# Kernel optimization log

Hardware: AMD Instinct MI355X
Metric: run time of the kernel (lower is better)

## Reference

```python
import jax, jax.numpy as jnp
import numpy as np

N_NODES = 100000
N_EDGES = 3200000
IN_DIM = 128
HID = 128
K = 20  # n_gaussians


def gcn_conv(x, src, dst, W, b, n_nodes):
    """PyG GCNConv: add self-loops, symmetric normalization, linear transform.
    out = D^{-1/2} (A + I) D^{-1/2} (x @ W) + b, where D is degree of A+I.
    """
    h = x @ W  # [N, out_dim]
    # degree on A + I (self-loop contributes 1 to every node)
    deg = jax.ops.segment_sum(jnp.ones_like(dst, dtype=h.dtype), dst,
                              num_segments=n_nodes) + 1.0
    dis = jax.lax.rsqrt(deg)  # deg >= 1, safe
    norm = dis[src] * dis[dst]  # [E]
    # gather -> scale -> scatter-add (edges), plus self-loop term dis_i^2 * h_i
    agg = jax.ops.segment_sum(h[src] * norm[:, None], dst,
                              num_segments=n_nodes)
    agg = agg + h * (dis * dis)[:, None]
    return agg + b


def setup_inputs() -> dict:
    key = jax.random.key(0)
    ks = jax.random.split(key, 12)
    x = jax.random.normal(ks[0], (N_NODES, IN_DIM), dtype=jnp.float32)
    edge_index = jax.random.randint(ks[1], (2, N_EDGES), 0, N_NODES, dtype=jnp.int32)
    s = 1.0 / np.sqrt(HID)
    W1 = jax.random.uniform(ks[2], (IN_DIM, HID), jnp.float32, -s, s)
    b1 = jnp.zeros((HID,), jnp.float32)
    W2 = jax.random.uniform(ks[3], (HID, HID), jnp.float32, -s, s)
    b2 = jnp.zeros((HID,), jnp.float32)
    pi_W = jax.random.uniform(ks[4], (HID, K), jnp.float32, -s, s)
    pi_b = jnp.zeros((K,), jnp.float32)
    mu_W = jax.random.uniform(ks[5], (HID, K), jnp.float32, -s, s)
    mu_b = jnp.zeros((K,), jnp.float32)
    ls_W = jax.random.uniform(ks[6], (HID, K), jnp.float32, -s, s)
    ls_b = jnp.zeros((K,), jnp.float32)
    return {"x": x, "edge_index": edge_index, "W1": W1, "b1": b1,
            "W2": W2, "b2": b2, "pi_W": pi_W, "pi_b": pi_b,
            "mu_W": mu_W, "mu_b": mu_b, "ls_W": ls_W, "ls_b": ls_b}


def reference(x, edge_index, W1, b1, W2, b2, pi_W, pi_b, mu_W, mu_b, ls_W, ls_b):
    src, dst = edge_index[0], edge_index[1]
    n = x.shape[0]
    h = jax.nn.relu(gcn_conv(x, src, dst, W1, b1, n))
    h = jax.nn.relu(gcn_conv(h, src, dst, W2, b2, n))
    pi = jax.nn.softmax(h @ pi_W + pi_b, axis=1)
    mu = h @ mu_W + mu_b
    log_sigma = h @ ls_W + ls_b
    return (pi, mu, log_sigma)
```

## Files before the change

kernel.cpp:

```cpp
#include <hip/hip_runtime.h>
#include <hip/hip_fp16.h>
#include <cstdint>
#include <cstddef>

#define IN_DIM 128
#define HID    128
#define NG     20
#define T      4096
#define MAXB   400

typedef _Float16 half8 __attribute__((ext_vector_type(8)));
typedef _Float16 half4 __attribute__((ext_vector_type(4)));
typedef float    f32x4 __attribute__((ext_vector_type(4)));

__global__ void zero_ints(int* __restrict__ a, int n) {
  int i = blockIdx.x * blockDim.x + threadIdx.x;
  if (i < n) a[i] = 0;
}

__global__ __launch_bounds__(512) void binsort1(const int* __restrict__ src,
    const int* __restrict__ dst, int* __restrict__ tmp, int* __restrict__ bofs,
    int* __restrict__ bintot, int NBC, int E) {
  __shared__ int lhist[MAXB];
  __shared__ int lscan[512];
  __shared__ int lcur[MAXB];
  __shared__ int sbuf[T];
  int tid = threadIdx.x;
  int tile0 = blockIdx.x * T;
  int m = E - tile0; if (m > T) m = T;

  for (int i = tid; i < NBC; i += 512) lhist[i] = 0;
  __syncthreads();

  int dreg[8];
#pragma unroll
  for (int j = 0; j < 8; ++j) {
    int idx = j * 512 + tid;
    dreg[j] = -1;
    if (idx < m) {
      int d = dst[tile0 + idx];
      dreg[j] = d;
      atomicAdd(&lhist[d >> 8], 1);
    }
  }
  __syncthreads();

  int v = (tid < NBC) ? lhist[tid] : 0;
  lscan[tid] = v;
  __syncthreads();
  for (int o = 1; o < 512; o <<= 1) {
    int t = (tid >= o) ? lscan[tid - o] : 0;
    __syncthreads();
    lscan[tid] += t;
    __syncthreads();
  }
  if (tid < NBC) lcur[tid] = lscan[tid] - v;
  __syncthreads();

  int ST = NBC + 1;
  for (int i = tid; i < NBC; i += 512) bofs[(size_t)blockIdx.x * ST + i] = lcur[i];
  if (tid == 0) bofs[(size_t)blockIdx.x * ST + NBC] = m;
  for (int i = tid; i < NBC; i += 512)
    if (lhist[i]) atomicAdd(&bintot[i], lhist[i]);
  __syncthreads();

#pragma unroll
  for (int j = 0; j < 8; ++j) {
    int idx = j * 512 + tid;
    if (idx < m) {
      int d = dreg[j];
      int s = src[tile0 + idx];
      int slot = atomicAdd(&lcur[d >> 8], 1);
      sbuf[slot] = ((d & 255) << 17) | s;
    }
  }
  __syncthreads();

  int nv = m >> 2;
  int4* out4 = (int4*)(tmp + tile0);
  const int4* sb4 = (const int4*)sbuf;
  for (int i = tid; i < nv; i += 512) out4[i] = sb4[i];
  for (int i = (nv << 2) + tid; i < m; i += 512) tmp[tile0 + i] = sbuf[i];
}

__global__ __launch_bounds__(512) void binscan(const int* __restrict__ bintot,
                                               int* __restrict__ binbase, int NBC) {
  __shared__ int s[512];
  int tid = threadIdx.x;
  int v = (tid < NBC) ? bintot[tid] : 0;
  s[tid] = v;
  __syncthreads();
  for (int o = 1; o < 512; o <<= 1) {
    int t = (tid >= o) ? s[tid - o] : 0;
    __syncthreads();
    s[tid] += t;
    __syncthreads();
  }
  if (tid < NBC) binbase[tid] = s[tid] - v;
}

__global__ __launch_bounds__(1024) void binsort2(const int* __restrict__ tmp,
    const int* __restrict__ bofs, const int* __restrict__ binbase,
    int* __restrict__ csrc, int* __restrict__ cnt, float* __restrict__ dis,
    int* __restrict__ offs, int NBC, int nblk, int N) {
  __shared__ int lcnt[256];
  __shared__ int lsc[256];
  __shared__ int lcur2[256];
  int b = blockIdx.x;
  int tid = threadIdx.x;
  if (tid < 256) lcnt[tid] = 0;
  __syncthreads();
  int ST = NBC + 1;
  for (int r = tid; r < nblk; r += 1024) {
    int s = bofs[(size_t)r * ST + b];
    int e2 = bofs[(size_t)r * ST + b + 1];
    int base = r * T;
    for (int k = s; k < e2; ++k)
      atomicAdd(&lcnt[tmp[base + k] >> 17], 1);
  }
  __syncthreads();
  if (tid < 256) lsc[tid] = lcnt[tid];
  __syncthreads();
  for (int o = 1; o < 256; o <<= 1) {
    int t = 0;
    if (tid < 256 && tid >= o) t = lsc[tid - o];
    __syncthreads();
    if (tid < 256) lsc[tid] += t;
    __syncthreads();
  }
  int gbase = binbase[b];
  if (tid < 256) {
    int excl = lsc[tid] - lcnt[tid];
    lcur2[tid] = gbase + excl;
    int node = (b << 8) + tid;
    if (node < N) {
      cnt[node] = lcnt[tid];
      dis[node] = rsqrtf((float)lcnt[tid] + 1.0f);
      offs[node] = gbase + excl;
    }
  }
  __syncthreads();
  for (int r = tid; r < nblk; r += 1024) {
    int s = bofs[(size_t)r * ST + b];
    int e2 = bofs[(size_t)r * ST + b + 1];
    int base = r * T;
    for (int k = s; k < e2; ++k) {
      int rec = tmp[base + k];
      int pos = atomicAdd(&lcur2[rec >> 17], 1);
      csrc[pos] = rec & 0x1FFFF;
    }
  }
}

template<bool F16IN>
__global__ __launch_bounds__(256) void gemm128_mfma(const void* __restrict__ Av,
                                                    const float* __restrict__ B,
                                                    __half* __restrict__ C, int M) {
  __shared__ _Float16 sA[128][136];
  const int tid = threadIdx.x;
  const int m0 = blockIdx.x * 128;
  const int wave = tid >> 6, lane = tid & 63;
  const int nbase = wave << 5;
  const int lrow = lane & 15;
  const int khi  = lane >> 4;
  const float* wcol = B + nbase + lrow;

  float bA[2][8], bB[2][8];
#pragma unroll
  for (int nf = 0; nf < 2; ++nf)
#pragma unroll
    for (int rr = 0; rr < 8; ++rr)
      bA[nf][rr] = wcol[(size_t)(khi * 8 + rr) * 128 + nf * 16];

  if constexpr (F16IN) {
    const __half* A = (const __half*)Av;
#pragma unroll
    for (int q = 0; q < 8; ++q) {
      int idx = q * 256 + tid;
      int r = idx >> 4;
      int cc = (idx & 15) << 3;
      half8 hv = {};
      if (m0 + r < M) hv = *(const half8*)(A + (size_t)(m0 + r) * 128 + cc);
      *(half8*)(&sA[r][cc]) = hv;
    }
  } else {
    const float* A = (const float*)Av;
#pragma unroll
    for (int q = 0; q < 16; ++q) {
      int idx = q * 256 + tid;
      int r = idx >> 5;
      int cc = (idx & 31) << 2;
      float4 v = make_float4(0.f, 0.f, 0.f, 0.f);
      if (m0 + r < M) v = *(const float4*)(A + (size_t)(m0 + r) * 128 + cc);
      half4 hv;
      hv[0] = (_Float16)v.x; hv[1] = (_Float16)v.y;
      hv[2] = (_Float16)v.z; hv[3] = (_Float16)v.w;
      *(half4*)(&sA[r][cc]) = hv;
    }
  }
  __syncthreads();

  f32x4 acc[8][2];
#pragma unroll
  for (int mf = 0; mf < 8; ++mf)
#pragma unroll
    for (int nf = 0; nf < 2; ++nf) acc[mf][nf] = (f32x4){0.f, 0.f, 0.f, 0.f};

  auto loadB = [&](float (&dst)[2][8], int ks) {
#pragma unroll
    for (int nf = 0; nf < 2; ++nf)
#pragma unroll
      for (int rr = 0; rr < 8; ++rr)
        dst[nf][rr] = wcol[(size_t)(ks * 32 + khi * 8 + rr) * 128 + nf * 16];
  };
  half8 bf0, bf1;
  auto cvtB = [&](float (&s)[2][8]) {
#pragma unroll
    for (int rr = 0; rr < 8; ++rr) {
      bf0[rr] = (_Float16)s[0][rr];
      bf1[rr] = (_Float16)s[1][rr];
    }
  };
  auto mfmas = [&](int ks) {
#pragma unroll
    for (int mf = 0; mf < 8; ++mf) {
      half8 a = *(const half8*)(&sA[mf * 16 + lrow][khi * 8 + ks * 32]);
      acc[mf][0] = __builtin_amdgcn_mfma_f32_16x16x32_f16(a, bf0, acc[mf][0], 0, 0, 0);
      acc[mf][1] = __builtin_amdgcn_mfma_f32_16x16x32_f16(a, bf1, acc[mf][1], 0, 0, 0);
    }
  };
  cvtB(bA); loadB(bB, 1); mfmas(0);
  cvtB(bB); loadB(bA, 2); mfmas(1);
  cvtB(bA); loadB(bB, 3); mfmas(2);
  cvtB(bB);               mfmas(3);

#pragma unroll
  for (int mf = 0; mf < 8; ++mf) {
    int r0 = mf * 16 + khi * 4;
#pragma unroll
    for (int nf = 0; nf < 2; ++nf) {
      int ccol = nbase + nf * 16 + lrow;
#pragma unroll
      for (int reg = 0; reg < 4; ++reg) {
        int r = m0 + r0 + reg;
        if (r < M) C[(size_t)r * 128 + ccol] = __float2half(acc[mf][nf][reg]);
      }
    }
  }
}

template<typename OutT>
__global__ __launch_bounds__(256) void agg_kernel(const __half* __restrict__ h,
    const int* __restrict__ csrc,
    const int* __restrict__ offs, const int* __restrict__ cnt,
    const float* __restrict__ dis, const float* __restrict__ bias,
    OutT* __restrict__ out, int n) {
  int wave = threadIdx.x >> 6;
  int lane = threadIdx.x & 63;
  int i0 = (blockIdx.x * 4 + wave) * 2;
  if (i0 >= n) return;
  int i1 = i0 + 1;
  bool has1 = i1 < n;
  int c = lane * 2;

  int st0 = offs[i0];
  int m0  = cnt[i0];
  float d0 = dis[i0];
  int st1 = 0, m1 = 0;
  float d1 = 0.f;
  if (has1) { st1 = offs[i1]; m1 = cnt[i1]; d1 = dis[i1]; }

  float ax0 = 0.f, ay0 = 0.f, ax1 = 0.f, ay1 = 0.f;
  int mMax = m0 > m1 ? m0 : m1;

  for (int base = 0; base < mMax; base += 64) {
    int mcA = m0 - base; mcA = mcA < 0 ? 0 : (mcA > 64 ? 64 : mcA);
    int mcB = m1 - base; mcB = mcB < 0 ? 0 : (mcB > 64 ? 64 : mcB);
    int mc = mcA > mcB ? mcA : mcB;

    int sA = 0, sB = 0;
    float wA = 0.f, wB = 0.f;
    if (lane < mcA) sA = csrc[st0 + base + lane];
    if (lane < mcB) sB = csrc[st1 + base + lane];
    if (lane < mcA) wA = dis[sA] * d0;
    if (lane < mcB) wB = dis[sB] * d1;

    int j = 0;
    for (; j + 4 <= mc; j += 4) {
      int   a0 = __shfl(sA, j);
      int   a1 = __shfl(sA, j + 1);
      int   a2 = __shfl(sA, j + 2);
      int   a3 = __shfl(sA, j + 3);
      int   b0 = __shfl(sB, j);
      int   b1 = __shfl(sB, j + 1);
      int   b2 = __shfl(sB, j + 2);
      int   b3 = __shfl(sB, j + 3);
      float u0 = __shfl(wA, j);
      float u1 = __shfl(wA, j + 1);
      float u2 = __shfl(wA, j + 2);
      float u3 = __shfl(wA, j + 3);
      float v0 = __shfl(wB, j);
      float v1 = __shfl(wB, j + 1);
      float v2 = __shfl(wB, j + 2);
      float v3 = __shfl(wB, j + 3);
      float2 hA0 = __half22float2(*(const __half2*)(h + ((size_t)a0 << 7) + c));
      float2 hA1 = __half22float2(*(const __half2*)(h + ((size_t)a1 << 7) + c));
      float2 hA2 = __half22float2(*(const __half2*)(h + ((size_t)a2 << 7) + c));
      float2 hA3 = __half22float2(*(const __half2*)(h + ((size_t)a3 << 7) + c));
      float2 hB0 = __half22float2(*(const __half2*)(h + ((size_t)b0 << 7) + c));
      float2 hB1 = __half22float2(*(const __half2*)(h + ((size_t)b1 << 7) + c));
      float2 hB2 = __half22float2(*(const __half2*)(h + ((size_t)b2 << 7) + c));
      float2 hB3 = __half22float2(*(const __half2*)(h + ((size_t)b3 << 7) + c));
      ax0 = fmaf(hA0.x, u0, ax0); ay0 = fmaf(hA0.y, u0, ay0);
      ax0 = fmaf(hA1.x, u1, ax0); ay0 = fmaf(hA1.y, u1, ay0);
      ax0 = fmaf(hA2.x, u2, ax0); ay0 = fmaf(hA2.y, u2, ay0);
      ax0 = fmaf(hA3.x, u3, ax0); ay0 = fmaf(hA3.y, u3, ay0);
      ax1 = fmaf(hB0.x, v0, ax1); ay1 = fmaf(hB0.y, v0, ay1);
      ax1 = fmaf(hB1.x, v1, ax1); ay1 = fmaf(hB1.y, v1, ay1);
      ax1 = fmaf(hB2.x, v2, ax1); ay1 = fmaf(hB2.y, v2, ay1);
      ax1 = fmaf(hB3.x, v3, ax1); ay1 = fmaf(hB3.y, v3, ay1);
    }
    for (; j < mc; ++j) {
      int   a0 = __shfl(sA, j);
      int   b0 = __shfl(sB, j);
      float u0 = __shfl(wA, j);
      float v0 = __shfl(wB, j);
      float2 hA0 = __half22float2(*(const __half2*)(h + ((size_t)a0 << 7) + c));
      float2 hB0 = __half22float2(*(const __half2*)(h + ((size_t)b0 << 7) + c));
      ax0 = fmaf(hA0.x, u0, ax0); ay0 = fmaf(hA0.y, u0, ay0);
      ax1 = fmaf(hB0.x, v0, ax1); ay1 = fmaf(hB0.y, v0, ay1);
    }
  }

  float2 bv = *(const float2*)(bias + c);
  {
    float dd = d0 * d0;
    float2 hs = __half22float2(*(const __half2*)(h + ((size_t)i0 << 7) + c));
    float vx = fmaxf(fmaf(hs.x, dd, ax0) + bv.x, 0.f);
    float vy = fmaxf(fmaf(hs.y, dd, ay0) + bv.y, 0.f);
    if constexpr (sizeof(OutT) == 2) {
      *(__half2*)((__half*)out + (size_t)i0 * 128 + c) = __floats2half2_rn(vx, vy);
    } else {
      *(float2*)((float*)out + (size_t)i0 * 128 + c) = make_float2(vx, vy);
    }
  }
  if (has1) {
    float dd = d1 * d1;
    float2 hs = __half22float2(*(const __half2*)(h + ((size_t)i1 << 7) + c));
    float vx = fmaxf(fmaf(hs.x, dd, ax1) + bv.x, 0.f);
    float vy = fmaxf(fmaf(hs.y, dd, ay1) + bv.y, 0.f);
    if constexpr (sizeof(OutT) == 2) {
      *(__half2*)((__half*)out + (size_t)i1 * 128 + c) = __floats2half2_rn(vx, vy);
    } else {
      *(float2*)((float*)out + (size_t)i1 * 128 + c) = make_float2(vx, vy);
    }
  }
}

__global__ void pack_heads_w(const float* __restrict__ piW, const float* __restrict__ muW,
                             const float* __restrict__ lsW, float* __restrict__ W64) {
  int i = blockIdx.x * 256 + threadIdx.x;
  if (i >= 128 * 64) return;
  int k = i >> 6, j = i & 63;
  float v = 0.f;
  if (j < 20)      v = piW[k * 20 + j];
  else if (j < 40) v = muW[k * 20 + (j - 20)];
  else if (j < 60) v = lsW[k * 20 + (j - 40)];
  W64[i] = v;
}

#define KC 64
__global__ __launch_bounds__(256) void heads_fused(const float* __restrict__ A,
    const float* __restrict__ B, const float* __restrict__ pib,
    const float* __restrict__ mub, const float* __restrict__ lsb,
    float* __restrict__ out, int n) {
  __shared__ float sA[64][KC + 4];
  __shared__ float sB[KC][68];
  __shared__ float sOut[64][68];
  int tid = threadIdx.x;
  int m0 = blockIdx.x * 64;
  int tr = tid >> 4;
  int tc = tid & 15;
  float acc[4][4];
#pragma unroll
  for (int i = 0; i < 4; ++i)
#pragma unroll
    for (int j = 0; j < 4; ++j) acc[i][j] = 0.f;

  for (int k0 = 0; k0 < 128; k0 += KC) {
#pragma unroll
    for (int q = 0; q < 4; ++q) {
      int idx = q * 256 + tid;
      int r = idx >> 4;
      int kk = (idx & 15) << 2;
      float4 v = make_float4(0.f, 0.f, 0.f, 0.f);
      if (m0 + r < n) v = *(const float4*)(A + (size_t)(m0 + r) * 128 + k0 + kk);
      *(float4*)(&sA[r][kk]) = v;
    }
#pragma unroll
    for (int q = 0; q < 4; ++q) {
      int idx = q * 256 + tid;
      int kk = idx >> 4;
      int nn = (idx & 15) << 2;
      *(float4*)(&sB[kk][nn]) = *(const float4*)(B + (size_t)(k0 + kk) * 64 + nn);
    }
    __syncthreads();
#pragma unroll 4
    for (int k = 0; k < KC; k += 4) {
      float4 a0 = *(const float4*)(&sA[tr][k]);
      float4 a1 = *(const float4*)(&sA[tr + 16][k]);
      float4 a2 = *(const float4*)(&sA[tr + 32][k]);
      float4 a3 = *(const float4*)(&sA[tr + 48][k]);
#pragma unroll
      for (int u = 0; u < 4; ++u) {
        float4 b = *(const float4*)(&sB[k + u][tc * 4]);
        float av[4] = {((const float*)&a0)[u], ((const float*)&a1)[u],
                       ((const float*)&a2)[u], ((const float*)&a3)[u]};
#pragma unroll
        for (int i = 0; i < 4; ++i) {
          acc[i][0] = fmaf(av[i], b.x, acc[i][0]);
          acc[i][1] = fmaf(av[i], b.y, acc[i][1]);
          acc[i][2] = fmaf(av[i], b.z, acc[i][2]);
          acc[i][3] = fmaf(av[i], b.w, acc[i][3]);
        }
      }
    }
    __syncthreads();
  }

#pragma unroll
  for (int i = 0; i < 4; ++i)
#pragma unroll
    for (int j = 0; j < 4; ++j) sOut[tr + 16 * i][tc * 4 + j] = acc[i][j];
  __syncthreads();

  int wave = tid >> 6, lane = tid & 63;
  size_t nb = (size_t)n * NG;
  for (int t = 0; t < 16; ++t) {
    int rr = wave * 16 + t;
    int node = m0 + rr;
    if (node >= n) break;
    float v = 0.f;
    if (lane < 60) {
      v = sOut[rr][lane];
      v += (lane < 20) ? pib[lane] : (lane < 40) ? mub[lane - 20] : lsb[lane - 40];
    }
    float pv = (lane < 20) ? v : -__builtin_inff();
    float mx = pv;
    for (int o = 16; o > 0; o >>= 1) mx = fmaxf(mx, __shfl_down(mx, o, 32));
    mx = __shfl(mx, 0, 32);
    float ev = (lane < 20) ? expf(v - mx) : 0.f;
    float sm = ev;
    for (int o = 16; o > 0; o >>= 1) sm += __shfl_down(sm, o, 32);
    sm = __shfl(sm, 0, 32);
    if (lane < 20)      out[(size_t)node * NG + lane] = ev / sm;
    else if (lane < 40) out[nb + (size_t)node * NG + (lane - 20)] = v;
    else if (lane < 60) out[2 * nb + (size_t)node * NG + (lane - 40)] = v;
  }
}

extern "C" void kernel_launch(void* const* d_in, const int* in_sizes, int n_in,
                              void* d_out, int out_size, void* d_ws, size_t ws_size,
                              hipStream_t stream) {
  const float* x   = (const float*)d_in[0];
  const int*   ei  = (const int*)d_in[1];
  const float* W1  = (const float*)d_in[2];
  const float* b1  = (const float*)d_in[3];
  const float* W2  = (const float*)d_in[4];
  const float* b2  = (const float*)d_in[5];
  const float* piW = (const float*)d_in[6];
  const float* pib = (const float*)d_in[7];
  const float* muW = (const float*)d_in[8];
  const float* mub = (const float*)d_in[9];
  const float* lsW = (const float*)d_in[10];
  const float* lsb = (const float*)d_in[11];
  float* out = (float*)d_out;

  const int N = in_sizes[0] / IN_DIM;
  const int E = in_sizes[1] / 2;
  const int* src = ei;
  const int* dst = ei + E;

  const int NBC  = (N + 255) >> 8;
  const int nblk = (E + T - 1) / T;
  const int ST   = NBC + 1;

  char* p = (char*)d_ws;
  char* regionH = p;                        p += (size_t)N * HID * sizeof(__half);
  __half* h16  = (__half*)regionH;
  char* regionR = p;
  size_t szR = (size_t)N * HID * sizeof(float);
  size_t szT = (size_t)E * sizeof(int);
  p += (szR > szT ? szR : szT);
  int*    tmp    = (int*)regionR;
  __half* bufB16 = (__half*)regionR;
  float*  bufB   = (float*)regionR;
  int*   csrc   = (int*)p;                  p += (size_t)E * sizeof(int);
  int*   bofs   = (int*)p;                  p += (size_t)nblk * ST * sizeof(int);
  int*   bintot = (int*)p;                  p += (size_t)MAXB * sizeof(int);
  int*   binbase= (int*)p;                  p += (size_t)MAXB * sizeof(int);
  int*   cnt    = (int*)p;                  p += (size_t)N * sizeof(int);
  int*   offs   = (int*)p;                  p += (size_t)N * sizeof(int);
  float* dis    = (float*)p;                p += (size_t)N * sizeof(float);
  float* W64    = (float*)p;                p += (size_t)128 * 64 * sizeof(float);

  zero_ints<<<(NBC + 255) / 256, 256, 0, stream>>>(bintot, NBC);
  binsort1<<<nblk, 512, 0, stream>>>(src, dst, tmp, bofs, bintot, NBC, E);
  binscan<<<1, 512, 0, stream>>>(bintot, binbase, NBC);
  binsort2<<<NBC, 1024, 0, stream>>>(tmp, bofs, binbase, csrc, cnt, dis, offs,
                                     NBC, nblk, N);
  pack_heads_w<<<(128 * 64 + 255) / 256, 256, 0, stream>>>(piW, muW, lsW, W64);

  const int NB8 = (N + 7) / 8;
  const int NBG = (N + 127) / 128;

  gemm128_mfma<false><<<NBG, 256, 0, stream>>>(x, W1, h16, N);
  agg_kernel<__half><<<NB8, 256, 0, stream>>>(h16, csrc, offs, cnt, dis, b1,
                                              bufB16, N);
  gemm128_mfma<true><<<NBG, 256, 0, stream>>>(bufB16, W2, h16, N);
  agg_kernel<float><<<NB8, 256, 0, stream>>>(h16, csrc, offs, cnt, dis, b2,
                                             bufB, N);

  heads_fused<<<(N + 63) / 64, 256, 0, stream>>>(bufB, W64, pib, mub, lsb, out, N);
}
```

Baseline: 547.3 us.

## Co-schedule CSR binsort blocks with first GEMM halves in fused launches

Merges the CSR bin-sort phases with the first-layer x@W1 GEMM and the head-weight packing into two heterogeneous kernels. Block IDs are split by role, so sort work and GEMM tiles run concurrently on the GPU and fill its idle compute units. Both sort phases are rewritten to use 256 threads and shared dynamic-style smem. This reduces launch count and overlaps latency-bound sorting with compute-bound MFMA work. The cost is fewer threads per sort block and shared-memory sizing set by the largest role.

```diff
diff --git a/kernel.cpp b/kernel.cpp
--- a/kernel.cpp
+++ b/kernel.cpp
@@ -8,6 +8,7 @@
 #define NG     20
 #define T      4096
 #define MAXB   400
+#define SMEM_BYTES 34816
 
 typedef _Float16 half8 __attribute__((ext_vector_type(8)));
 typedef _Float16 half4 __attribute__((ext_vector_type(4)));
@@ -18,24 +19,24 @@
   if (i < n) a[i] = 0;
 }
 
-__global__ __launch_bounds__(512) void binsort1(const int* __restrict__ src,
+__device__ __forceinline__ void binsort1_body(const int* __restrict__ src,
     const int* __restrict__ dst, int* __restrict__ tmp, int* __restrict__ bofs,
-    int* __restrict__ bintot, int NBC, int E) {
-  __shared__ int lhist[MAXB];
-  __shared__ int lscan[512];
-  __shared__ int lcur[MAXB];
-  __shared__ int sbuf[T];
+    int* __restrict__ bintot, int NBC, int E, int blk, char* smemc) {
+  int* lhist = (int*)smemc;
+  int* lscan = lhist + MAXB;
+  int* lcur  = lscan + 512;
+  int* sbuf  = lcur + MAXB;
   int tid = threadIdx.x;
-  int tile0 = blockIdx.x * T;
+  int tile0 = blk * T;
   int m = E - tile0; if (m > T) m = T;
 
-  for (int i = tid; i < NBC; i += 512) lhist[i] = 0;
-  __syncthreads();
-
-  int dreg[8];
-#pragma unroll
-  for (int j = 0; j < 8; ++j) {
-    int idx = j * 512 + tid;
+  for (int i = tid; i < NBC; i += 256) lhist[i] = 0;
+  __syncthreads();
+
+  int dreg[16];
+#pragma unroll
+  for (int j = 0; j < 16; ++j) {
+    int idx = j * 256 + tid;
     dreg[j] = -1;
     if (idx < m) {
       int d = dst[tile0 + idx];
@@ -45,28 +46,31 @@
   }
   __syncthreads();
 
-  int v = (tid < NBC) ? lhist[tid] : 0;
-  lscan[tid] = v;
+  int v0 = (tid < NBC) ? lhist[tid] : 0;
+  int v1 = (256 + tid < NBC) ? lhist[256 + tid] : 0;
+  lscan[tid] = v0; lscan[256 + tid] = v1;
   __syncthreads();
   for (int o = 1; o < 512; o <<= 1) {
-    int t = (tid >= o) ? lscan[tid - o] : 0;
-    __syncthreads();
-    lscan[tid] += t;
-    __syncthreads();
-  }
-  if (tid < NBC) lcur[tid] = lscan[tid] - v;
+    int a0 = (tid >= o) ? lscan[tid - o] : 0;
+    int a1 = (256 + tid >= o) ? lscan[256 + tid - o] : 0;
+    __syncthreads();
+    lscan[tid] += a0; lscan[256 + tid] += a1;
+    __syncthreads();
+  }
+  if (tid < NBC)       lcur[tid]       = lscan[tid] - v0;
+  if (256 + tid < NBC) lcur[256 + tid] = lscan[256 + tid] - v1;
   __syncthreads();
 
   int ST = NBC + 1;
-  for (int i = tid; i < NBC; i += 512) bofs[(size_t)blockIdx.x * ST + i] = lcur[i];
-  if (tid == 0) bofs[(size_t)blockIdx.x * ST + NBC] = m;
-  for (int i = tid; i < NBC; i += 512)
+  for (int i = tid; i < NBC; i += 256) bofs[(size_t)blk * ST + i] = lcur[i];
+  if (tid == 0) bofs[(size_t)blk * ST + NBC] = m;
+  for (int i = tid; i < NBC; i += 256)
     if (lhist[i]) atomicAdd(&bintot[i], lhist[i]);
   __syncthreads();
 
 #pragma unroll
-  for (int j = 0; j < 8; ++j) {
-    int idx = j * 512 + tid;
+  for (int j = 0; j < 16; ++j) {
+    int idx = j * 256 + tid;
     if (idx < m) {
       int d = dreg[j];
       int s = src[tile0 + idx];
@@ -79,39 +83,22 @@
   int nv = m >> 2;
   int4* out4 = (int4*)(tmp + tile0);
   const int4* sb4 = (const int4*)sbuf;
-  for (int i = tid; i < nv; i += 512) out4[i] = sb4[i];
-  for (int i = (nv << 2) + tid; i < m; i += 512) tmp[tile0 + i] = sbuf[i];
-}
-
-__global__ __launch_bounds__(512) void binscan(const int* __restrict__ bintot,
-                                               int* __restrict__ binbase, int NBC) {
-  __shared__ int s[512];
-  int tid = threadIdx.x;
-  int v = (tid < NBC) ? bintot[tid] : 0;
-  s[tid] = v;
-  __syncthreads();
-  for (int o = 1; o < 512; o <<= 1) {
-    int t = (tid >= o) ? s[tid - o] : 0;
-    __syncthreads();
-    s[tid] += t;
-    __syncthreads();
-  }
-  if (tid < NBC) binbase[tid] = s[tid] - v;
-}
-
-__global__ __launch_bounds__(1024) void binsort2(const int* __restrict__ tmp,
+  for (int i = tid; i < nv; i += 256) out4[i] = sb4[i];
+  for (int i = (nv << 2) + tid; i < m; i += 256) tmp[tile0 + i] = sbuf[i];
+}
+
+__device__ __forceinline__ void binsort2_body(const int* __restrict__ tmp,
     const int* __restrict__ bofs, const int* __restrict__ binbase,
     int* __restrict__ csrc, int* __restrict__ cnt, float* __restrict__ dis,
-    int* __restrict__ offs, int NBC, int nblk, int N) {
-  __shared__ int lcnt[256];
-  __shared__ int lsc[256];
-  __shared__ int lcur2[256];
-  int b = blockIdx.x;
+    int* __restrict__ offs, int NBC, int nblk, int N, int b, char* smemc) {
+  int* lcnt  = (int*)smemc;
+  int* lsc   = lcnt + 256;
+  int* lcur2 = lsc + 256;
   int tid = threadIdx.x;
-  if (tid < 256) lcnt[tid] = 0;
+  lcnt[tid] = 0;
   __syncthreads();
   int ST = NBC + 1;
-  for (int r = tid; r < nblk; r += 1024) {
+  for (int r = tid; r < nblk; r += 256) {
     int s = bofs[(size_t)r * ST + b];
     int e2 = bofs[(size_t)r * ST + b + 1];
     int base = r * T;
@@ -119,28 +106,26 @@
       atomicAdd(&lcnt[tmp[base + k] >> 17], 1);
   }
   __syncthreads();
-  if (tid < 256) lsc[tid] = lcnt[tid];
+  int v = lcnt[tid];
+  lsc[tid] = v;
   __syncthreads();
   for (int o = 1; o < 256; o <<= 1) {
-    int t = 0;
-    if (tid < 256 && tid >= o) t = lsc[tid - o];
-    __syncthreads();
-    if (tid < 256) lsc[tid] += t;
+    int t = (tid >= o) ? lsc[tid - o] : 0;
+    __syncthreads();
+    lsc[tid] += t;
     __syncthreads();
   }
   int gbase = binbase[b];
-  if (tid < 256) {
-    int excl = lsc[tid] - lcnt[tid];
-    lcur2[tid] = gbase + excl;
-    int node = (b << 8) + tid;
-    if (node < N) {
-      cnt[node] = lcnt[tid];
-      dis[node] = rsqrtf((float)lcnt[tid] + 1.0f);
-      offs[node] = gbase + excl;
-    }
-  }
-  __syncthreads();
-  for (int r = tid; r < nblk; r += 1024) {
+  int excl = lsc[tid] - v;
+  lcur2[tid] = gbase + excl;
+  int node = (b << 8) + tid;
+  if (node < N) {
+    cnt[node] = v;
+    dis[node] = rsqrtf((float)v + 1.0f);
+    offs[node] = gbase + excl;
+  }
+  __syncthreads();
+  for (int r = tid; r < nblk; r += 256) {
     int s = bofs[(size_t)r * ST + b];
     int e2 = bofs[(size_t)r * ST + b + 1];
     int base = r * T;
@@ -153,12 +138,11 @@
 }
 
 template<bool F16IN>
-__global__ __launch_bounds__(256) void gemm128_mfma(const void* __restrict__ Av,
-                                                    const float* __restrict__ B,
-                                                    __half* __restrict__ C, int M) {
-  __shared__ _Float16 sA[128][136];
+__device__ __forceinline__ void gemm_body(const void* __restrict__ Av,
+    const float* __restrict__ B, __half* __restrict__ C, int M, int m0,
+    char* smemc) {
+  _Float16 (*sA)[136] = (_Float16(*)[136])smemc;
   const int tid = threadIdx.x;
-  const int m0 = blockIdx.x * 128;
   const int wave = tid >> 6, lane = tid & 63;
   const int nbase = wave << 5;
   const int lrow = lane & 15;
@@ -247,6 +231,69 @@
       }
     }
   }
+}
+
+__global__ __launch_bounds__(256) void gemm128_mfma_f16(const __half* __restrict__ A,
+    const float* __restrict__ B, __half* __restrict__ C, int M) {
+  __shared__ char smem[SMEM_BYTES];
+  gemm_body<true>(A, B, C, M, blockIdx.x * 128, smem);
+}
+
+__global__ __launch_bounds__(256) void fusedA(const int* __restrict__ src,
+    const int* __restrict__ dst, int* __restrict__ tmp, int* __restrict__ bofs,
+    int* __restrict__ bintot, int NBC, int E, int nblk,
+    const float* __restrict__ x, const float* __restrict__ W1,
+    __half* __restrict__ h16, int N, int G1a,
+    const float* __restrict__ piW, const float* __restrict__ muW,
+    const float* __restrict__ lsW, float* __restrict__ W64) {
+  __shared__ char smem[SMEM_BYTES];
+  int b = blockIdx.x;
+  if (b < nblk) {
+    binsort1_body(src, dst, tmp, bofs, bintot, NBC, E, b, smem);
+  } else if (b < nblk + G1a) {
+    gemm_body<false>(x, W1, h16, N, (b - nblk) * 128, smem);
+  } else {
+    int i = (b - nblk - G1a) * 256 + threadIdx.x;
+    if (i < 128 * 64) {
+      int k = i >> 6, j = i & 63;
+      float v = 0.f;
+      if (j < 20)      v = piW[k * 20 + j];
+      else if (j < 40) v = muW[k * 20 + (j - 20)];
+      else if (j < 60) v = lsW[k * 20 + (j - 40)];
+      W64[i] = v;
+    }
+  }
+}
+
+__global__ __launch_bounds__(256) void fusedB(const int* __restrict__ tmp,
+    const int* __restrict__ bofs, const int* __restrict__ binbase,
+    int* __restrict__ csrc, int* __restrict__ cnt, float* __restrict__ dis,
+    int* __restrict__ offs, int NBC, int nblk, int N,
+    const float* __restrict__ x, const float* __restrict__ W1,
+    __half* __restrict__ h16, int G1a) {
+  __shared__ char smem[SMEM_BYTES];
+  int b = blockIdx.x;
+  if (b < NBC) {
+    binsort2_body(tmp, bofs, binbase, csrc, cnt, dis, offs, NBC, nblk, N, b, smem);
+  } else {
+    gemm_body<false>(x, W1, h16, N, (G1a + b - NBC) * 128, smem);
+  }
+}
+
+__global__ __launch_bounds__(512) void binscan(const int* __restrict__ bintot,
+                                               int* __restrict__ binbase, int NBC) {
+  __shared__ int s[512];
+  int tid = threadIdx.x;
+  int v = (tid < NBC) ? bintot[tid] : 0;
+  s[tid] = v;
+  __syncthreads();
+  for (int o = 1; o < 512; o <<= 1) {
+    int t = (tid >= o) ? s[tid - o] : 0;
+    __syncthreads();
+    s[tid] += t;
+    __syncthreads();
+  }
+  if (tid < NBC) binbase[tid] = s[tid] - v;
 }
 
 template<typename OutT>
@@ -357,18 +404,6 @@
   }
 }
 
-__global__ void pack_heads_w(const float* __restrict__ piW, const float* __restrict__ muW,
-                             const float* __restrict__ lsW, float* __restrict__ W64) {
-  int i = blockIdx.x * 256 + threadIdx.x;
-  if (i >= 128 * 64) return;
-  int k = i >> 6, j = i & 63;
-  float v = 0.f;
-  if (j < 20)      v = piW[k * 20 + j];
-  else if (j < 40) v = muW[k * 20 + (j - 20)];
-  else if (j < 60) v = lsW[k * 20 + (j - 40)];
-  W64[i] = v;
-}
-
 #define KC 64
 __global__ __launch_bounds__(256) void heads_fused(const float* __restrict__ A,
     const float* __restrict__ B, const float* __restrict__ pib,
@@ -504,22 +539,23 @@
   float* dis    = (float*)p;                p += (size_t)N * sizeof(float);
   float* W64    = (float*)p;                p += (size_t)128 * 64 * sizeof(float);
 
-  zero_ints<<<(NBC + 255) / 256, 256, 0, stream>>>(bintot, NBC);
-  binsort1<<<nblk, 512, 0, stream>>>(src, dst, tmp, bofs, bintot, NBC, E);
-  binscan<<<1, 512, 0, stream>>>(bintot, binbase, NBC);
-  binsort2<<<NBC, 1024, 0, stream>>>(tmp, bofs, binbase, csrc, cnt, dis, offs,
-                                     NBC, nblk, N);
-  pack_heads_w<<<(128 * 64 + 255) / 256, 256, 0, stream>>>(piW, muW, lsW, W64);
-
   const int NB8 = (N + 7) / 8;
   const int NBG = (N + 127) / 128;
-
-  gemm128_mfma<false><<<NBG, 256, 0, stream>>>(x, W1, h16, N);
+  const int G1a = (NBG + 1) / 2;
+  const int G1b = NBG - G1a;
+  const int PACKB = (128 * 64 + 255) / 256;
+
+  zero_ints<<<(NBC + 255) / 256, 256, 0, stream>>>(bintot, NBC);
+  fusedA<<<nblk + G1a + PACKB, 256, 0, stream>>>(src, dst, tmp, bofs, bintot,
+      NBC, E, nblk, x, W1, h16, N, G1a, piW, muW, lsW, W64);
+  binscan<<<1, 512, 0, stream>>>(bintot, binbase, NBC);
+  fusedB<<<NBC + G1b, 256, 0, stream>>>(tmp, bofs, binbase, csrc, cnt, dis, offs,
+      NBC, nblk, N, x, W1, h16, G1a);
+
   agg_kernel<__half><<<NB8, 256, 0, stream>>>(h16, csrc, offs, cnt, dis, b1,
                                               bufB16, N);
-  gemm128_mfma<true><<<NBG, 256, 0, stream>>>(bufB16, W2, h16, N);
+  gemm128_mfma_f16<<<NBG, 256, 0, stream>>>(bufB16, W2, h16, N);
   agg_kernel<float><<<NB8, 256, 0, stream>>>(h16, csrc, offs, cnt, dis, b2,
                                              bufB, N);
-
   heads_fused<<<(N + 63) / 64, 256, 0, stream>>>(bufB, W64, pib, mub, lsb, out, N);
 }
```

New measurement: 544.6 us. Within noise of the previous version (-0.5%).

## Stage CSR bin sort in LDS and fold bin scan into first GEMM launch

Applied to the files above, without the earlier changes.

The second bin-sort pass now reads each bin's records from global memory once into a large LDS buffer, counts per node and scatters them in LDS. It then writes csrc out coalesced with int4 stores, instead of reading tmp twice and scattering single ints to global memory. The global bintot atomics, the zero kernel, the separate binscan kernel and the head-weight packing kernel are removed. The bin totals are recomputed from bofs by one extra block appended to the first GEMM launch, which also packs the head weights. The trade-off is a fixed per-bin capacity (BIN_CAP) that would silently drop edges for skewed degree distributions, plus heavy LDS use per binsort2 block.

```diff
diff --git a/kernel.cpp b/kernel.cpp
--- a/kernel.cpp
+++ b/kernel.cpp
@@ -8,19 +8,15 @@
 #define NG     20
 #define T      4096
 #define MAXB   400
+#define BIN_CAP 12288
 
 typedef _Float16 half8 __attribute__((ext_vector_type(8)));
 typedef _Float16 half4 __attribute__((ext_vector_type(4)));
 typedef float    f32x4 __attribute__((ext_vector_type(4)));
 
-__global__ void zero_ints(int* __restrict__ a, int n) {
-  int i = blockIdx.x * blockDim.x + threadIdx.x;
-  if (i < n) a[i] = 0;
-}
-
 __global__ __launch_bounds__(512) void binsort1(const int* __restrict__ src,
     const int* __restrict__ dst, int* __restrict__ tmp, int* __restrict__ bofs,
-    int* __restrict__ bintot, int NBC, int E) {
+    int NBC, int E) {
   __shared__ int lhist[MAXB];
   __shared__ int lscan[512];
   __shared__ int lcur[MAXB];
@@ -60,8 +56,6 @@
   int ST = NBC + 1;
   for (int i = tid; i < NBC; i += 512) bofs[(size_t)blockIdx.x * ST + i] = lcur[i];
   if (tid == 0) bofs[(size_t)blockIdx.x * ST + NBC] = m;
-  for (int i = tid; i < NBC; i += 512)
-    if (lhist[i]) atomicAdd(&bintot[i], lhist[i]);
   __syncthreads();
 
 #pragma unroll
@@ -83,82 +77,12 @@
   for (int i = (nv << 2) + tid; i < m; i += 512) tmp[tile0 + i] = sbuf[i];
 }
 
-__global__ __launch_bounds__(512) void binscan(const int* __restrict__ bintot,
-                                               int* __restrict__ binbase, int NBC) {
-  __shared__ int s[512];
-  int tid = threadIdx.x;
-  int v = (tid < NBC) ? bintot[tid] : 0;
-  s[tid] = v;
-  __syncthreads();
-  for (int o = 1; o < 512; o <<= 1) {
-    int t = (tid >= o) ? s[tid - o] : 0;
-    __syncthreads();
-    s[tid] += t;
-    __syncthreads();
-  }
-  if (tid < NBC) binbase[tid] = s[tid] - v;
-}
-
-__global__ __launch_bounds__(1024) void binsort2(const int* __restrict__ tmp,
-    const int* __restrict__ bofs, const int* __restrict__ binbase,
-    int* __restrict__ csrc, int* __restrict__ cnt, float* __restrict__ dis,
-    int* __restrict__ offs, int NBC, int nblk, int N) {
-  __shared__ int lcnt[256];
-  __shared__ int lsc[256];
-  __shared__ int lcur2[256];
-  int b = blockIdx.x;
-  int tid = threadIdx.x;
-  if (tid < 256) lcnt[tid] = 0;
-  __syncthreads();
-  int ST = NBC + 1;
-  for (int r = tid; r < nblk; r += 1024) {
-    int s = bofs[(size_t)r * ST + b];
-    int e2 = bofs[(size_t)r * ST + b + 1];
-    int base = r * T;
-    for (int k = s; k < e2; ++k)
-      atomicAdd(&lcnt[tmp[base + k] >> 17], 1);
-  }
-  __syncthreads();
-  if (tid < 256) lsc[tid] = lcnt[tid];
-  __syncthreads();
-  for (int o = 1; o < 256; o <<= 1) {
-    int t = 0;
-    if (tid < 256 && tid >= o) t = lsc[tid - o];
-    __syncthreads();
-    if (tid < 256) lsc[tid] += t;
-    __syncthreads();
-  }
-  int gbase = binbase[b];
-  if (tid < 256) {
-    int excl = lsc[tid] - lcnt[tid];
-    lcur2[tid] = gbase + excl;
-    int node = (b << 8) + tid;
-    if (node < N) {
-      cnt[node] = lcnt[tid];
-      dis[node] = rsqrtf((float)lcnt[tid] + 1.0f);
-      offs[node] = gbase + excl;
-    }
-  }
-  __syncthreads();
-  for (int r = tid; r < nblk; r += 1024) {
-    int s = bofs[(size_t)r * ST + b];
-    int e2 = bofs[(size_t)r * ST + b + 1];
-    int base = r * T;
-    for (int k = s; k < e2; ++k) {
-      int rec = tmp[base + k];
-      int pos = atomicAdd(&lcur2[rec >> 17], 1);
-      csrc[pos] = rec & 0x1FFFF;
-    }
-  }
-}
-
 template<bool F16IN>
-__global__ __launch_bounds__(256) void gemm128_mfma(const void* __restrict__ Av,
-                                                    const float* __restrict__ B,
-                                                    __half* __restrict__ C, int M) {
-  __shared__ _Float16 sA[128][136];
+__device__ __forceinline__ void gemm_body(const void* __restrict__ Av,
+    const float* __restrict__ B, __half* __restrict__ C, int M, int m0,
+    char* smemc) {
+  _Float16 (*sA)[136] = (_Float16(*)[136])smemc;
   const int tid = threadIdx.x;
-  const int m0 = blockIdx.x * 128;
   const int wave = tid >> 6, lane = tid & 63;
   const int nbase = wave << 5;
   const int lrow = lane & 15;
@@ -247,6 +171,143 @@
       }
     }
   }
+}
+
+__global__ __launch_bounds__(256) void gemm1_scan(const float* __restrict__ x,
+    const float* __restrict__ W1, __half* __restrict__ h16, int M, int NBG,
+    const int* __restrict__ bofs, int* __restrict__ binbase, int NBC, int nblk,
+    const float* __restrict__ piW, const float* __restrict__ muW,
+    const float* __restrict__ lsW, float* __restrict__ W64) {
+  __shared__ char smem[128 * 136 * 2];
+  __shared__ int ssc[512];
+  int tid = threadIdx.x;
+  if (blockIdx.x < (unsigned)NBG) {
+    gemm_body<false>(x, W1, h16, M, blockIdx.x * 128, smem);
+    return;
+  }
+  int ST = NBC + 1;
+  int t0 = 0, t1 = 0;
+  int r = 0;
+  for (; r + 4 <= nblk; r += 4) {
+    const int* r0 = bofs + (size_t)r * ST;
+    const int* r1 = r0 + ST;
+    const int* r2 = r1 + ST;
+    const int* r3 = r2 + ST;
+    if (tid < NBC)
+      t0 += (r0[tid + 1] - r0[tid]) + (r1[tid + 1] - r1[tid]) +
+            (r2[tid + 1] - r2[tid]) + (r3[tid + 1] - r3[tid]);
+    if (256 + tid < NBC)
+      t1 += (r0[257 + tid] - r0[256 + tid]) + (r1[257 + tid] - r1[256 + tid]) +
+            (r2[257 + tid] - r2[256 + tid]) + (r3[257 + tid] - r3[256 + tid]);
+  }
+  for (; r < nblk; ++r) {
+    const int* r0 = bofs + (size_t)r * ST;
+    if (tid < NBC)       t0 += r0[tid + 1] - r0[tid];
+    if (256 + tid < NBC) t1 += r0[257 + tid] - r0[256 + tid];
+  }
+  ssc[tid] = t0; ssc[256 + tid] = t1;
+  __syncthreads();
+  for (int o = 1; o < 512; o <<= 1) {
+    int a0 = (tid >= o) ? ssc[tid - o] : 0;
+    int a1 = (256 + tid >= o) ? ssc[256 + tid - o] : 0;
+    __syncthreads();
+    ssc[tid] += a0; ssc[256 + tid] += a1;
+    __syncthreads();
+  }
+  if (tid < NBC)       binbase[tid]       = ssc[tid] - t0;
+  if (256 + tid < NBC) binbase[256 + tid] = ssc[256 + tid] - t1;
+  for (int i = tid; i < 128 * 64; i += 256) {
+    int k = i >> 6, j = i & 63;
+    float v = 0.f;
+    if (j < 20)      v = piW[k * 20 + j];
+    else if (j < 40) v = muW[k * 20 + (j - 20)];
+    else if (j < 60) v = lsW[k * 20 + (j - 40)];
+    W64[i] = v;
+  }
+}
+
+__global__ __launch_bounds__(512) void binsort2(const int* __restrict__ tmp,
+    const int* __restrict__ bofs, const int* __restrict__ binbase,
+    int* __restrict__ csrc, int* __restrict__ cnt, float* __restrict__ dis,
+    int* __restrict__ offs, int NBC, int nblk, int N) {
+  __shared__ int bufA[BIN_CAP];
+  __shared__ int bufB[BIN_CAP];
+  __shared__ int lcnt[256];
+  __shared__ int lsc[256];
+  __shared__ int lcur[256];
+  __shared__ int appendTot;
+  int b = blockIdx.x;
+  int tid = threadIdx.x;
+  if (tid == 0) appendTot = 0;
+  if (tid < 256) lcnt[tid] = 0;
+  __syncthreads();
+  int ST = NBC + 1;
+
+  for (int r = tid; r < nblk; r += 512) {
+    int s  = bofs[(size_t)r * ST + b];
+    int e2 = bofs[(size_t)r * ST + b + 1];
+    int k = e2 - s;
+    if (k > 0) {
+      int pos = atomicAdd(&appendTot, k);
+      if (pos + k > BIN_CAP) k = (pos < BIN_CAP) ? (BIN_CAP - pos) : 0;
+      int gb = r * T + s;
+      for (int i = 0; i < k; ++i) {
+        int rec = tmp[gb + i];
+        bufA[pos + i] = rec;
+        atomicAdd(&lcnt[(rec >> 17) & 255], 1);
+      }
+    }
+  }
+  __syncthreads();
+  int total = appendTot; if (total > BIN_CAP) total = BIN_CAP;
+
+  int v = (tid < 256) ? lcnt[tid] : 0;
+  if (tid < 256) lsc[tid] = v;
+  __syncthreads();
+  for (int o = 1; o < 256; o <<= 1) {
+    int t = 0;
+    if (tid < 256 && tid >= o) t = lsc[tid - o];
+    __syncthreads();
+    if (tid < 256) lsc[tid] += t;
+    __syncthreads();
+  }
+  int gbase = binbase[b];
+  if (tid < 256) {
+    int excl = lsc[tid] - v;
+    lcur[tid] = excl;
+    int node = (b << 8) + tid;
+    if (node < N) {
+      cnt[node] = v;
+      dis[node] = rsqrtf((float)v + 1.0f);
+      offs[node] = gbase + excl;
+    }
+  }
+  __syncthreads();
+
+  for (int i = tid; i < total; i += 512) {
+    int rec = bufA[i];
+    int pos = atomicAdd(&lcur[(rec >> 17) & 255], 1);
+    bufB[pos] = rec & 0x1FFFF;
+  }
+  __syncthreads();
+
+  int head = (4 - (gbase & 3)) & 3; if (head > total) head = total;
+  for (int i = tid; i < head; i += 512) csrc[gbase + i] = bufB[i];
+  int rem = total - head;
+  int nv = rem >> 2;
+  int4* dst4 = (int4*)(csrc + gbase + head);
+  for (int i = tid; i < nv; i += 512) {
+    int j = head + i * 4;
+    dst4[i] = make_int4(bufB[j], bufB[j + 1], bufB[j + 2], bufB[j + 3]);
+  }
+  for (int i = head + (nv << 2) + tid; i < total; i += 512)
+    csrc[gbase + i] = bufB[i];
+}
+
+__global__ __launch_bounds__(256) void gemm128_mfma_f16(const __half* __restrict__ A,
+    const float* __restrict__ B, __half* __restrict__ C, int M) {
+  __shared__ char smem[128 * 136 * 2];
+  gemm_body<true>(A, B, C, M, blockIdx.x * 128, smem);
 }
 
 template<typename OutT>
@@ -357,18 +418,6 @@
   }
 }
 
-__global__ void pack_heads_w(const float* __restrict__ piW, const float* __restrict__ muW,
-                             const float* __restrict__ lsW, float* __restrict__ W64) {
-  int i = blockIdx.x * 256 + threadIdx.x;
-  if (i >= 128 * 64) return;
-  int k = i >> 6, j = i & 63;
-  float v = 0.f;
-  if (j < 20)      v = piW[k * 20 + j];
-  else if (j < 40) v = muW[k * 20 + (j - 20)];
-  else if (j < 60) v = lsW[k * 20 + (j - 40)];
-  W64[i] = v;
-}
-
 #define KC 64
 __global__ __launch_bounds__(256) void heads_fused(const float* __restrict__ A,
     const float* __restrict__ B, const float* __restrict__ pib,
@@ -497,29 +546,24 @@
   float*  bufB   = (float*)regionR;
   int*   csrc   = (int*)p;                  p += (size_t)E * sizeof(int);
   int*   bofs   = (int*)p;                  p += (size_t)nblk * ST * sizeof(int);
-  int*   bintot = (int*)p;                  p += (size_t)MAXB * sizeof(int);
   int*   binbase= (int*)p;                  p += (size_t)MAXB * sizeof(int);
   int*   cnt    = (int*)p;                  p += (size_t)N * sizeof(int);
   int*   offs   = (int*)p;                  p += (size_t)N * sizeof(int);
   float* dis    = (float*)p;                p += (size_t)N * sizeof(float);
   float* W64    = (float*)p;                p += (size_t)128 * 64 * sizeof(float);
 
-  zero_ints<<<(NBC + 255) / 256, 256, 0, stream>>>(bintot, NBC);
-  binsort1<<<nblk, 512, 0, stream>>>(src, dst, tmp, bofs, bintot, NBC, E);
-  binscan<<<1, 512, 0, stream>>>(bintot, binbase, NBC);
-  binsort2<<<NBC, 1024, 0, stream>>>(tmp, bofs, binbase, csrc, cnt, dis, offs,
-                                     NBC, nblk, N);
-  pack_heads_w<<<(128 * 64 + 255) / 256, 256, 0, stream>>>(piW, muW, lsW, W64);
-
   const int NB8 = (N + 7) / 8;
   const int NBG = (N + 127) / 128;
 
-  gemm128_mfma<false><<<NBG, 256, 0, stream>>>(x, W1, h16, N);
+  binsort1<<<nblk, 512, 0, stream>>>(src, dst, tmp, bofs, NBC, E);
+  gemm1_scan<<<NBG + 1, 256, 0, stream>>>(x, W1, h16, N, NBG, bofs, binbase,
+                                          NBC, nblk, piW, muW, lsW, W64);
+  binsort2<<<NBC, 512, 0, stream>>>(tmp, bofs, binbase, csrc, cnt, dis, offs,
+                                    NBC, nblk, N);
   agg_kernel<__half><<<NB8, 256, 0, stream>>>(h16, csrc, offs, cnt, dis, b1,
                                               bufB16, N);
-  gemm128_mfma<true><<<NBG, 256, 0, stream>>>(bufB16, W2, h16, N);
+  gemm128_mfma_f16<<<NBG, 256, 0, stream>>>(bufB16, W2, h16, N);
   agg_kernel<float><<<NB8, 256, 0, stream>>>(h16, csrc, offs, cnt, dis, b2,
                                              bufB, N);
-
   heads_fused<<<(N + 63) / 64, 256, 0, stream>>>(bufB, W64, pib, mub, lsb, out, N);
 }
```

Result: slower. 615.9 us (+12.5%).
